# Performance work log

Hardware: AMD Instinct MI355X
Metric: run time of the kernel (lower is better)

## Reference

```python
import jax, jax.numpy as jnp
import numpy as np

D_MODEL = 2048
N_HEADS = 16
KV_HEADS = 4
HEAD_DIM = D_MODEL // N_HEADS            # 128
GROUP = N_HEADS // KV_HEADS              # 4
KV_WIDTH = KV_HEADS * HEAD_DIM           # 512
B, T = 2, 2048


def setup_inputs() -> dict:
    key = jax.random.key(0)
    ks = jax.random.split(key, 5)
    s = 0.02
    x = jax.random.normal(ks[0], (B, T, D_MODEL), dtype=jnp.float32)
    attn_mask = jnp.tril(jnp.ones((T, T), dtype=bool))  # causal
    qkv_w = jax.random.normal(ks[1], (D_MODEL, D_MODEL + 2 * KV_WIDTH), dtype=jnp.float32) * s
    qkv_b = jax.random.normal(ks[2], (D_MODEL + 2 * KV_WIDTH,), dtype=jnp.float32) * s
    proj_w = jax.random.normal(ks[3], (D_MODEL, D_MODEL), dtype=jnp.float32) * s
    proj_b = jax.random.normal(ks[4], (D_MODEL,), dtype=jnp.float32) * s
    return {"x": x, "attn_mask": attn_mask, "qkv_w": qkv_w, "qkv_b": qkv_b,
            "proj_w": proj_w, "proj_b": proj_b}


def reference(x, attn_mask, qkv_w, qkv_b, proj_w, proj_b):
    b, t, c = x.shape
    qkv = x @ qkv_w + qkv_b                               # [b,t,3072]
    q = qkv[..., :D_MODEL]
    k = qkv[..., D_MODEL:D_MODEL + KV_WIDTH]
    v = qkv[..., D_MODEL + KV_WIDTH:]
    # q: [b, kv_heads, group, t, d]; k,v: [b, kv_heads, t, d]
    q = q.reshape(b, t, KV_HEADS, GROUP, HEAD_DIM).transpose(0, 2, 3, 1, 4)
    k = k.reshape(b, t, KV_HEADS, HEAD_DIM).transpose(0, 2, 1, 3)
    v = v.reshape(b, t, KV_HEADS, HEAD_DIM).transpose(0, 2, 1, 3)
    scale = 1.0 / jnp.sqrt(jnp.asarray(HEAD_DIM, dtype=x.dtype))
    att = jnp.einsum('bkgtd,bksd->bkgts', q, k) * scale   # [b,kv,g,t,t]
    att = jnp.where(attn_mask, att, jnp.asarray(-jnp.inf, dtype=att.dtype))
    att = jax.nn.softmax(att, axis=-1)
    out = jnp.einsum('bkgts,bksd->bkgtd', att, v)         # [b,kv,g,t,d]
    out = out.transpose(0, 3, 1, 2, 4).reshape(b, t, c)
    return out @ proj_w + proj_b
```

## Files before the change

### kernel.cpp

```cpp
#include <hip/hip_runtime.h>
#include <cstdint>
#include <cstddef>

#define D_MODEL 2048
#define T_SEQ   2048
#define BATCH   2
#define N_HEADS 16
#define KV_HEADS 4
#define HEAD_DIM 128
#define QKV_N   3072
#define ROWS    (BATCH * T_SEQ)

typedef float  floatx4 __attribute__((ext_vector_type(4)));
typedef short  shortx8 __attribute__((ext_vector_type(8)));
typedef __bf16 bf16x8  __attribute__((ext_vector_type(8)));

typedef const void __attribute__((address_space(1))) gvoid_t;
typedef void __attribute__((address_space(3)))       svoid_t;

__device__ __forceinline__ floatx4 mfma16(shortx8 a, shortx8 b, floatx4 c) {
  return __builtin_amdgcn_mfma_f32_16x16x32_bf16(
      __builtin_bit_cast(bf16x8, a), __builtin_bit_cast(bf16x8, b), c, 0, 0, 0);
}

__device__ __forceinline__ unsigned short f2bf(float f) {
  union { float f; unsigned int u; } v; v.f = f;
  unsigned int u = v.u;
  u += 0x7fffu + ((u >> 16) & 1u);
  return (unsigned short)(u >> 16);
}

__device__ __forceinline__ unsigned short f2bf_hw(float f) {
  return __builtin_bit_cast(unsigned short, (__bf16)f);
}

__device__ __forceinline__ unsigned int pk2bf(float lo, float hi) {
  return (unsigned int)f2bf_hw(lo) | ((unsigned int)f2bf_hw(hi) << 16);
}

__global__ __launch_bounds__(256) void prep_kernel(
    const float* __restrict__ x, unsigned short* __restrict__ x_bf,
    const float* __restrict__ qkv_w, unsigned short* __restrict__ qkvw_t,
    const float* __restrict__ proj_w, unsigned short* __restrict__ projw_t)
{
  __shared__ float tile[32][33];
  const int bid = blockIdx.x, tid = threadIdx.x;
  if (bid < 8192) {
    const int i = bid * 256 + tid;
    float4 v = ((const float4*)x)[i];
    ushort4 o;
    o.x = f2bf(v.x); o.y = f2bf(v.y); o.z = f2bf(v.z); o.w = f2bf(v.w);
    ((ushort4*)x_bf)[i] = o;
    return;
  }
  const float* W; unsigned short* Wt; int N, bx, by;
  if (bid < 14336) { const int v = bid - 8192;  W = qkv_w;  Wt = qkvw_t;  N = QKV_N;   bx = v % 96; by = v / 96; }
  else             { const int v = bid - 14336; W = proj_w; Wt = projw_t; N = D_MODEL; bx = v % 64; by = v / 64; }
  const int K = D_MODEL;
  const int n0 = bx * 32, k0 = by * 32;
  const int tx = tid & 31, ty = tid >> 5;
  #pragma unroll
  for (int i = 0; i < 32; i += 8)
    tile[ty + i][tx] = W[(size_t)(k0 + ty + i) * N + n0 + tx];
  __syncthreads();
  #pragma unroll
  for (int i = 0; i < 32; i += 8)
    Wt[(size_t)(n0 + ty + i) * K + k0 + tx] = f2bf(tile[tx][ty + i]);
}

template<int NB, int SWZ>
__global__ __launch_bounds__(512, 2) void gemm256(
    const unsigned short* __restrict__ A,
    const unsigned short* __restrict__ Bt,
    const float* __restrict__ bias,
    void* __restrict__ Cout,
    unsigned short* __restrict__ kst,
    unsigned short* __restrict__ vst,
    int M, int N, int K, int cmode)
{
  __shared__ __align__(16) unsigned short lds[32768 + NB * 16384];
  const int tid  = threadIdx.x;
  const int wave = tid >> 6, lane = tid & 63;
  const int quad = lane >> 4, l16 = lane & 15;
  const int wr = wave >> 2, wc = wave & 3;

  int bm, bn;
  if (SWZ) {
    const int nwg = gridDim.x * gridDim.y;
    const int cpx = nwg >> 3;
    const int f   = blockIdx.y * gridDim.x + blockIdx.x;
    const int w   = (f & 7) * cpx + (f >> 3);
    bm = (w / gridDim.x) * 256;
    bn = (w % gridDim.x) * (NB * 128);
  } else {
    bm = blockIdx.y * 256;
    bn = blockIdx.x * (NB * 128);
  }
  const int NT = K >> 6;

  const int r0 = tid >> 3;
  const int cx = (tid & 7) ^ (r0 & 7);
  const size_t K64 = (size_t)64 * K;
  const unsigned short* a_src = A  + (size_t)(bm + r0) * K + cx * 8;
  const unsigned short* b_src = Bt + (size_t)(bn + r0) * K + cx * 8;
  const int wOff = wave * 512;

  #define LDSA_(buf, half) (lds + (((buf) << 1) + (half)) * 8192)
  #define LDSB_(buf, half) (lds + 32768 + (((buf) << 1) + (half)) * (NB * 4096))
  #define KOFFA(h, t) ((size_t)(h) * 128 * K + (size_t)(t) * 64)
  #define KOFFB(h, t) ((size_t)(h) * (64 * NB) * K + (size_t)(t) * 64)
  #define STAGE_A(srcbase, ldshalf, koff) do {                                        \
    __builtin_amdgcn_global_load_lds((gvoid_t*)((srcbase) + (koff)),                  \
        (svoid_t*)((ldshalf) + wOff), 16, 0, 0);                                      \
    __builtin_amdgcn_global_load_lds((gvoid_t*)((srcbase) + (koff) + K64),            \
        (svoid_t*)((ldshalf) + wOff + 4096), 16, 0, 0);                               \
  } while (0)
  #define STAGE_B(srcbase, ldshalf, koff) do {                                        \
    _Pragma("unroll")                                                                 \
    for (int j_ = 0; j_ < NB; ++j_)                                                   \
      __builtin_amdgcn_global_load_lds(                                               \
          (gvoid_t*)((srcbase) + (koff) + (size_t)j_ * K64),                          \
          (svoid_t*)((ldshalf) + wOff + j_ * 4096), 16, 0, 0);                        \
  } while (0)

  const int rowA = (wr * 64 + l16) * 64;
  const int rowB = (wc * (16 * NB) + l16) * 64;
  const int xo0 = ((quad)     ^ (l16 & 7)) * 8;
  const int xo1 = ((4 + quad) ^ (l16 & 7)) * 8;

  floatx4 acc[8][2 * NB] = {};
  shortx8 Afr[4][2];
  shortx8 Bfr[2 * NB][2];

  STAGE_A(a_src, LDSA_(0, 0), KOFFA(0, 0));
  STAGE_B(b_src, LDSB_(0, 0), KOFFB(0, 0));
  STAGE_B(b_src, LDSB_(0, 1), KOFFB(1, 0));
  STAGE_A(a_src, LDSA_(0, 1), KOFFA(1, 0));
  if (NT > 1) {
    STAGE_A(a_src, LDSA_(1, 0), KOFFA(0, 1));
    STAGE_B(b_src, LDSB_(1, 0), KOFFB(0, 1));
    STAGE_B(b_src, LDSB_(1, 1), KOFFB(1, 1));
  }

  for (int t = 0; t < NT; ++t) {
    const int buf = t & 1;
    unsigned short* sA0 = LDSA_(buf, 0);
    unsigned short* sA1 = LDSA_(buf, 1);
    unsigned short* sB0 = LDSB_(buf, 0);
    unsigned short* sB1 = LDSB_(buf, 1);

    if (t == NT - 1) asm volatile("s_waitcnt vmcnt(0)" ::: "memory");
    else if constexpr (NB == 2) asm volatile("s_waitcnt vmcnt(6)" ::: "memory");
    else                        asm volatile("s_waitcnt vmcnt(4)" ::: "memory");
    __builtin_amdgcn_s_barrier();
    #pragma unroll
    for (int mi = 0; mi < 4; ++mi) {
      Afr[mi][0] = *(const shortx8*)(sA0 + rowA + mi * 1024 + xo0);
      Afr[mi][1] = *(const shortx8*)(sA0 + rowA + mi * 1024 + xo1);
    }
    #pragma unroll
    for (int ni = 0; ni < NB; ++ni) {
      Bfr[ni][0] = *(const shortx8*)(sB0 + rowB + ni * 1024 + xo0);
      Bfr[ni][1] = *(const shortx8*)(sB0 + rowB + ni * 1024 + xo1);
    }
    if (t + 1 < NT) STAGE_A(a_src, LDSA_(buf ^ 1, 1), KOFFA(1, t + 1));
    asm volatile("s_waitcnt lgkmcnt(0)" ::: "memory");
    __builtin_amdgcn_s_setprio(1);
    #pragma unroll
    for (int ks = 0; ks < 2; ++ks)
      #pragma unroll
      for (int mi = 0; mi < 4; ++mi)
        #pragma unroll
        for (int ni = 0; ni < NB; ++ni)
          acc[mi][ni] = mfma16(Afr[mi][ks], Bfr[ni][ks], acc[mi][ni]);
    __builtin_amdgcn_s_setprio(0);
    __builtin_amdgcn_s_barrier();

    #pragma unroll
    for (int ni = 0; ni < NB; ++ni) {
      Bfr[NB + ni][0] = *(const shortx8*)(sB1 + rowB + ni * 1024 + xo0);
      Bfr[NB + ni][1] = *(const shortx8*)(sB1 + rowB + ni * 1024 + xo1);
    }
    if (t + 2 < NT) STAGE_A(a_src, LDSA_(buf, 0), KOFFA(0, t + 2));
    __builtin_amdgcn_s_barrier();
    asm volatile("s_waitcnt lgkmcnt(0)" ::: "memory");
    __builtin_amdgcn_s_setprio(1);
    #pragma unroll
    for (int ks = 0; ks < 2; ++ks)
      #pragma unroll
      for (int mi = 0; mi < 4; ++mi)
        #pragma unroll
        for (int ni = 0; ni < NB; ++ni)
          acc[mi][NB + ni] = mfma16(Afr[mi][ks], Bfr[NB + ni][ks], acc[mi][NB + ni]);
    __builtin_amdgcn_s_setprio(0);
    __builtin_amdgcn_s_barrier();

    #pragma unroll
    for (int mi = 0; mi < 4; ++mi) {
      Afr[mi][0] = *(const shortx8*)(sA1 + rowA + mi * 1024 + xo0);
      Afr[mi][1] = *(const shortx8*)(sA1 + rowA + mi * 1024 + xo1);
    }
    if (t + 2 < NT) STAGE_B(b_src, LDSB_(buf, 0), KOFFB(0, t + 2));
    __builtin_amdgcn_s_barrier();
    asm volatile("s_waitcnt lgkmcnt(0)" ::: "memory");
    __builtin_amdgcn_s_setprio(1);
    #pragma unroll
    for (int ks = 0; ks < 2; ++ks)
      #pragma unroll
      for (int mi = 0; mi < 4; ++mi)
        #pragma unroll
        for (int ni = 0; ni < NB; ++ni)
          acc[4 + mi][NB + ni] = mfma16(Afr[mi][ks], Bfr[NB + ni][ks], acc[4 + mi][NB + ni]);
    __builtin_amdgcn_s_setprio(0);
    __builtin_amdgcn_s_barrier();

    if (t + 2 < NT) STAGE_B(b_src, LDSB_(buf, 1), KOFFB(1, t + 2));
    __builtin_amdgcn_s_barrier();
    __builtin_amdgcn_s_setprio(1);
    #pragma unroll
    for (int ks = 0; ks < 2; ++ks)
      #pragma unroll
      for (int mi = 0; mi < 4; ++mi)
        #pragma unroll
        for (int ni = 0; ni < NB; ++ni)
          acc[4 + mi][ni] = mfma16(Afr[mi][ks], Bfr[ni][ks], acc[4 + mi][ni]);
    __builtin_amdgcn_s_setprio(0);
    __builtin_amdgcn_s_barrier();
  }

  #pragma unroll
  for (int mi = 0; mi < 8; ++mi) {
    const int row = bm + (mi >> 2) * 128 + wr * 64 + (mi & 3) * 16 + quad * 4;
    #pragma unroll
    for (int ni = 0; ni < 2 * NB; ++ni) {
      const int col = bn + (ni / NB) * (64 * NB) + wc * (16 * NB) + (ni % NB) * 16 + l16;
      const float bv = bias[col];
      #pragma unroll
      for (int r = 0; r < 4; ++r) {
        float v = acc[mi][ni][r] + bv;
        if (cmode == 0) {
          ((float*)Cout)[(size_t)(row + r) * N + col] = v;
        } else {
          const unsigned short h = f2bf_hw(v);
          const int rw = row + r;
          const int t = rw & 2047, bb = rw >> 11;
          if (col < 2048) {
            ((unsigned short*)Cout)[(size_t)rw * 2048 + col] = h;
          } else if (col < 2560) {
            const int c2 = col - 2048, kvh = c2 >> 7, d = c2 & 127;
            kst[((((size_t)bb * 4 + kvh) * 16 + (d >> 3)) * 2048 + t) * 8 + (d & 7)] = h;
          } else {
            const int c2 = col - 2560, kvh = c2 >> 7, d = c2 & 127;
            const int ts = (t & ~31) | (((t >> 2) & 3) << 3) | (((t >> 4) & 1) << 2) | (t & 3);
            vst[((((size_t)bb * 4 + kvh) * 256 + (ts >> 3)) * 128 + d) * 8 + (ts & 7)] = h;
          }
        }
      }
    }
  }
  #undef LDSA_
  #undef LDSB_
  #undef KOFFA
  #undef KOFFB
  #undef STAGE_A
  #undef STAGE_B
}

__global__ __launch_bounds__(512, 4) void attn_kernel(
    const unsigned short* __restrict__ qbuf,
    const unsigned short* __restrict__ kst,
    const unsigned short* __restrict__ vst,
    unsigned short* __restrict__ aout)
{
  __shared__ __align__(16) unsigned short sK[2][16 * 64 * 8];
  __shared__ __align__(16) unsigned short sV[2][8 * 128 * 8];

  const int tid  = threadIdx.x;
  const int wave = tid >> 6, lane = tid & 63;
  const int split = wave >> 2, g = wave & 3;
  const int quad = lane >> 4, l16 = lane & 15;
  const int head = blockIdx.y, b = blockIdx.z;
  const int kvh = head >> 2;
  const float cf = 0.08838834764831845f * 1.4426950408889634f;
  const float THR = 25.0f;

  const unsigned short* kbase = kst + (size_t)((b * KV_HEADS + kvh) * 16) * 2048 * 8;
  const unsigned short* vbase = vst + (size_t)((b * KV_HEADS + kvh) * 256) * 128 * 8;

  float* mrgO  = (float*)&sK[0][0];
  float* mrgML = (float*)&sV[0][0];

  #define STAGE_KV(sp, kb_) do {                                               \
    _Pragma("unroll")                                                          \
    for (int it_ = 0; it_ < 4; ++it_) {                                        \
      const int c_ = it_ * 4 + g;                                              \
      __builtin_amdgcn_global_load_lds(                                        \
          (gvoid_t*)(kbase + ((size_t)c_ * 2048 + (kb_)) * 8 + lane * 8),      \
          (svoid_t*)(&sK[sp][c_ * 512]), 16, 0, 0);                            \
    }                                                                          \
    const unsigned short* vt_ = vbase + (size_t)((kb_) >> 3) * 128 * 8;        \
    _Pragma("unroll")                                                          \
    for (int it_ = 0; it_ < 4; ++it_) {                                        \
      const int c_ = it_ * 4 + g;                                              \
      __builtin_amdgcn_global_load_lds(                                        \
          (gvoid_t*)(vt_ + c_ * 512 + lane * 8),                               \
          (svoid_t*)(&sV[sp][c_ * 512]), 16, 0, 0);                            \
    }                                                                          \
  } while (0)

  #pragma unroll 1
  for (int half = 0; half < 2; ++half) {
    const int qt = half ? blockIdx.x : (31 - blockIdx.x);
    const int q0 = qt * 64;

    shortx8 qf[4];
    {
      const unsigned short* qp = qbuf + (size_t)(b * T_SEQ + q0 + g * 16 + l16) * 2048
                                 + head * HEAD_DIM + quad * 8;
      #pragma unroll
      for (int ks = 0; ks < 4; ++ks)
        qf[ks] = *(const shortx8*)(qp + ks * 32);
    }

    float m_i = -__builtin_inff(), l_i = 0.f;
    floatx4 o_acc[8] = {};

    const int J = (qt >> 1) + 1;
    for (int j = 0; j < J; ++j) {
      const int kt = 2 * j + split;
      const bool act = (kt <= qt);
      floatx4 st[4] = {};
      unsigned int pk[4][2];

      __builtin_amdgcn_s_barrier();
      if (act) STAGE_KV(split, kt * 64);
      asm volatile("s_waitcnt vmcnt(4)" ::: "memory");
      __builtin_amdgcn_s_barrier();

      if (act) {
        __builtin_amdgcn_s_setprio(1);
        #pragma unroll
        for (int ks = 0; ks < 4; ++ks) {
          #pragma unroll
          for (int ct = 0; ct < 4; ++ct) {
            shortx8 kf = *(const shortx8*)&sK[split][((ks * 4 + quad) * 64 + ct * 16 + l16) * 8];
            st[ct] = mfma16(kf, qf[ks], st[ct]);
          }
        }
        __builtin_amdgcn_s_setprio(0);

        if (kt == qt) {
          const int qrow = q0 + g * 16 + l16;
          const int kb = kt * 64;
          #pragma unroll
          for (int ct = 0; ct < 4; ++ct) {
            #pragma unroll
            for (int r = 0; r < 4; ++r)
              if (kb + ct * 16 + quad * 4 + r > qrow) st[ct][r] = -__builtin_inff();
          }
        }

        float lmx = -__builtin_inff();
        #pragma unroll
        for (int ct = 0; ct < 4; ++ct)
          lmx = fmaxf(lmx, fmaxf(fmaxf(st[ct][0], st[ct][1]), fmaxf(st[ct][2], st[ct][3])));
        if (__ballot(lmx > m_i + THR)) {
          float m = lmx;
          m = fmaxf(m, __shfl_xor(m, 16));
          m = fmaxf(m, __shfl_xor(m, 32));
          const float newm = fmaxf(m_i, m);
          const float alpha = exp2f((m_i - newm) * cf);
          m_i = newm;
          l_i *= alpha;
          #pragma unroll
          for (int nt = 0; nt < 8; ++nt)
            #pragma unroll
            for (int r = 0; r < 4; ++r) o_acc[nt][r] *= alpha;
        }

        const float nmc = m_i * cf;
        float ps = 0.f;
        #pragma unroll
        for (int ct = 0; ct < 4; ++ct) {
          #pragma unroll
          for (int r = 0; r < 4; ++r) {
            st[ct][r] = exp2f(fmaf(st[ct][r], cf, -nmc));
            ps += st[ct][r];
          }
          pk[ct][0] = pk2bf(st[ct][0], st[ct][1]);
          pk[ct][1] = pk2bf(st[ct][2], st[ct][3]);
        }
        l_i += ps;
      }

      asm volatile("s_waitcnt vmcnt(0)" ::: "memory");
      __builtin_amdgcn_s_barrier();

      if (act) {
        #pragma unroll
        for (int kc = 0; kc < 2; ++kc) {
          union { unsigned int u[4]; shortx8 s; } pa;
          pa.u[0] = pk[2 * kc][0];     pa.u[1] = pk[2 * kc][1];
          pa.u[2] = pk[2 * kc + 1][0]; pa.u[3] = pk[2 * kc + 1][1];
          __builtin_amdgcn_s_setprio(1);
          #pragma unroll
          for (int nt = 0; nt < 8; ++nt) {
            shortx8 vf = *(const shortx8*)&sV[split][((kc * 4 + quad) * 128 + nt * 16 + l16) * 8];
            o_acc[nt] = mfma16(vf, pa.s, o_acc[nt]);
          }
          __builtin_amdgcn_s_setprio(0);
        }
      }
    }

    __builtin_amdgcn_s_barrier();
    if (split == 1) {
      #pragma unroll
      for (int nt = 0; nt < 8; ++nt)
        #pragma unroll
        for (int r = 0; r < 4; ++r)
          mrgO[g * 2048 + (nt * 16 + quad * 4 + r) * 16 + l16] = o_acc[nt][r];
      mrgML[(g * 64 + lane) * 2]     = m_i;
      mrgML[(g * 64 + lane) * 2 + 1] = l_i;
    }
    asm volatile("s_waitcnt lgkmcnt(0)" ::: "memory");
    __builtin_amdgcn_s_barrier();

    if (split == 0) {
      const float m1 = mrgML[(g * 64 + lane) * 2];
      const float l1 = mrgML[(g * 64 + lane) * 2 + 1];
      const float M  = fmaxf(m_i, m1);
      const float a0 = exp2f((m_i - M) * cf);
      const float a1 = exp2f((m1 - M) * cf);
      float lm = a0 * l_i + a1 * l1;
      #pragma unroll
      for (int nt = 0; nt < 8; ++nt)
        #pragma unroll
        for (int r = 0; r < 4; ++r)
          o_acc[nt][r] = a0 * o_acc[nt][r]
                       + a1 * mrgO[g * 2048 + (nt * 16 + quad * 4 + r) * 16 + l16];

      lm += __shfl_xor(lm, 16);
      lm += __shfl_xor(lm, 32);
      const float inv = 1.f / lm;
      const size_t orow = (size_t)(b * T_SEQ + q0 + g * 16 + l16) * D_MODEL + head * HEAD_DIM;
      #pragma unroll
      for (int nt = 0; nt < 8; ++nt) {
        uint2 w2;
        w2.x = pk2bf(o_acc[nt][0] * inv, o_acc[nt][1] * inv);
        w2.y = pk2bf(o_acc[nt][2] * inv, o_acc[nt][3] * inv);
        *(uint2*)&aout[orow + nt * 16 + quad * 4] = w2;
      }
    }
  }
  #undef STAGE_KV
}

extern "C" void kernel_launch(void* const* d_in, const int* in_sizes, int n_in,
                              void* d_out, int out_size, void* d_ws, size_t ws_size,
                              hipStream_t stream) {
  const float* x      = (const float*)d_in[0];
  const float* qkv_w  = (const float*)d_in[2];
  const float* qkv_b  = (const float*)d_in[3];
  const float* proj_w = (const float*)d_in[4];
  const float* proj_b = (const float*)d_in[5];
  float* out = (float*)d_out;

  char* ws = (char*)d_ws;
  unsigned short* x_bf    = (unsigned short*)(ws);
  unsigned short* qkvw_t  = (unsigned short*)(ws + (size_t)16777216);
  unsigned short* projw_t = (unsigned short*)(ws + (size_t)29360128);
  unsigned short* qbuf    = (unsigned short*)(ws + (size_t)37748736);
  unsigned short* kstaged = (unsigned short*)(ws + (size_t)54525952);
  unsigned short* vstaged = (unsigned short*)(ws + (size_t)58720256);
  unsigned short* attn_out = x_bf;

  prep_kernel<<<18432, 256, 0, stream>>>(x, x_bf, qkv_w, qkvw_t, proj_w, projw_t);
  gemm256<2, 1><<<dim3(QKV_N / 256, ROWS / 256), 512, 0, stream>>>(
      x_bf, qkvw_t, qkv_b, (void*)qbuf, kstaged, vstaged, ROWS, QKV_N, D_MODEL, 2);
  attn_kernel<<<dim3(16, N_HEADS, BATCH), 512, 0, stream>>>(qbuf, kstaged, vstaged, attn_out);
  gemm256<1, 0><<<dim3(D_MODEL / 128, ROWS / 256), 512, 0, stream>>>(
      attn_out, projw_t, proj_b, (void*)out, nullptr, nullptr, ROWS, D_MODEL, D_MODEL, 0);
}
```

Baseline: 294.2 us.

## Simplify GEMM LDS pipeline to whole-tile double buffering with one barrier

Replaces the fine-grained half-tile staging schedule with a plain double-buffer scheme. Each iteration now waits for all outstanding global-to-LDS loads, issues one barrier, and prefetches the whole next K-tile into the other buffer. The aim is to cut the many per-iteration barriers and explicit lgkmcnt waits. In exchange, prefetch depth drops from about one and a half tiles to one, and vmcnt(0) waits for every load each iteration, which risks exposing global memory latency.

```diff
diff --git a/kernel.cpp b/kernel.cpp
--- a/kernel.cpp
+++ b/kernel.cpp
@@ -122,6 +122,12 @@
           (gvoid_t*)((srcbase) + (koff) + (size_t)j_ * K64),                          \
           (svoid_t*)((ldshalf) + wOff + j_ * 4096), 16, 0, 0);                        \
   } while (0)
+  #define STAGE_TILE(bf_, tt_) do {                                                   \
+    STAGE_A(a_src, LDSA_(bf_, 0), KOFFA(0, tt_));                                     \
+    STAGE_A(a_src, LDSA_(bf_, 1), KOFFA(1, tt_));                                     \
+    STAGE_B(b_src, LDSB_(bf_, 0), KOFFB(0, tt_));                                     \
+    STAGE_B(b_src, LDSB_(bf_, 1), KOFFB(1, tt_));                                     \
+  } while (0)
 
   const int rowA = (wr * 64 + l16) * 64;
   const int rowB = (wc * (16 * NB) + l16) * 64;
@@ -132,15 +138,7 @@
   shortx8 Afr[4][2];
   shortx8 Bfr[2 * NB][2];
 
-  STAGE_A(a_src, LDSA_(0, 0), KOFFA(0, 0));
-  STAGE_B(b_src, LDSB_(0, 0), KOFFB(0, 0));
-  STAGE_B(b_src, LDSB_(0, 1), KOFFB(1, 0));
-  STAGE_A(a_src, LDSA_(0, 1), KOFFA(1, 0));
-  if (NT > 1) {
-    STAGE_A(a_src, LDSA_(1, 0), KOFFA(0, 1));
-    STAGE_B(b_src, LDSB_(1, 0), KOFFB(0, 1));
-    STAGE_B(b_src, LDSB_(1, 1), KOFFB(1, 1));
-  }
+  STAGE_TILE(0, 0);
 
   for (int t = 0; t < NT; ++t) {
     const int buf = t & 1;
@@ -149,10 +147,10 @@
     unsigned short* sB0 = LDSB_(buf, 0);
     unsigned short* sB1 = LDSB_(buf, 1);
 
-    if (t == NT - 1) asm volatile("s_waitcnt vmcnt(0)" ::: "memory");
-    else if constexpr (NB == 2) asm volatile("s_waitcnt vmcnt(6)" ::: "memory");
-    else                        asm volatile("s_waitcnt vmcnt(4)" ::: "memory");
+    asm volatile("s_waitcnt vmcnt(0)" ::: "memory");
     __builtin_amdgcn_s_barrier();
+    if (t + 1 < NT) STAGE_TILE(buf ^ 1, t + 1);
+
     #pragma unroll
     for (int mi = 0; mi < 4; ++mi) {
       Afr[mi][0] = *(const shortx8*)(sA0 + rowA + mi * 1024 + xo0);
@@ -163,8 +161,6 @@
       Bfr[ni][0] = *(const shortx8*)(sB0 + rowB + ni * 1024 + xo0);
       Bfr[ni][1] = *(const shortx8*)(sB0 + rowB + ni * 1024 + xo1);
     }
-    if (t + 1 < NT) STAGE_A(a_src, LDSA_(buf ^ 1, 1), KOFFA(1, t + 1));
-    asm volatile("s_waitcnt lgkmcnt(0)" ::: "memory");
     __builtin_amdgcn_s_setprio(1);
     #pragma unroll
     for (int ks = 0; ks < 2; ++ks)
@@ -174,16 +170,12 @@
         for (int ni = 0; ni < NB; ++ni)
           acc[mi][ni] = mfma16(Afr[mi][ks], Bfr[ni][ks], acc[mi][ni]);
     __builtin_amdgcn_s_setprio(0);
-    __builtin_amdgcn_s_barrier();
 
     #pragma unroll
     for (int ni = 0; ni < NB; ++ni) {
       Bfr[NB + ni][0] = *(const shortx8*)(sB1 + rowB + ni * 1024 + xo0);
       Bfr[NB + ni][1] = *(const shortx8*)(sB1 + rowB + ni * 1024 + xo1);
     }
-    if (t + 2 < NT) STAGE_A(a_src, LDSA_(buf, 0), KOFFA(0, t + 2));
-    __builtin_amdgcn_s_barrier();
-    asm volatile("s_waitcnt lgkmcnt(0)" ::: "memory");
     __builtin_amdgcn_s_setprio(1);
     #pragma unroll
     for (int ks = 0; ks < 2; ++ks)
@@ -193,16 +185,12 @@
         for (int ni = 0; ni < NB; ++ni)
           acc[mi][NB + ni] = mfma16(Afr[mi][ks], Bfr[NB + ni][ks], acc[mi][NB + ni]);
     __builtin_amdgcn_s_setprio(0);
-    __builtin_amdgcn_s_barrier();
 
     #pragma unroll
     for (int mi = 0; mi < 4; ++mi) {
       Afr[mi][0] = *(const shortx8*)(sA1 + rowA + mi * 1024 + xo0);
       Afr[mi][1] = *(const shortx8*)(sA1 + rowA + mi * 1024 + xo1);
     }
-    if (t + 2 < NT) STAGE_B(b_src, LDSB_(buf, 0), KOFFB(0, t + 2));
-    __builtin_amdgcn_s_barrier();
-    asm volatile("s_waitcnt lgkmcnt(0)" ::: "memory");
     __builtin_amdgcn_s_setprio(1);
     #pragma unroll
     for (int ks = 0; ks < 2; ++ks)
@@ -212,10 +200,7 @@
         for (int ni = 0; ni < NB; ++ni)
           acc[4 + mi][NB + ni] = mfma16(Afr[mi][ks], Bfr[NB + ni][ks], acc[4 + mi][NB + ni]);
     __builtin_amdgcn_s_setprio(0);
-    __builtin_amdgcn_s_barrier();
-
-    if (t + 2 < NT) STAGE_B(b_src, LDSB_(buf, 1), KOFFB(1, t + 2));
-    __builtin_amdgcn_s_barrier();
+
     __builtin_amdgcn_s_setprio(1);
     #pragma unroll
     for (int ks = 0; ks < 2; ++ks)
@@ -225,7 +210,6 @@
         for (int ni = 0; ni < NB; ++ni)
           acc[4 + mi][ni] = mfma16(Afr[mi][ks], Bfr[ni][ks], acc[4 + mi][ni]);
     __builtin_amdgcn_s_setprio(0);
-    __builtin_amdgcn_s_barrier();
   }
 
   #pragma unroll
@@ -264,6 +248,7 @@
   #undef KOFFB
   #undef STAGE_A
   #undef STAGE_B
+  #undef STAGE_TILE
 }
 
 __global__ __launch_bounds__(512, 4) void attn_kernel(
```

Result: no change. 289.1 us (-1.7%).
